# Kernel tuning notes

Hardware: AMD Instinct MI355X
Metric: run time of the kernel (lower is better)

## Reference

```python
import jax, jax.numpy as jnp
import numpy as np

N, C_IN, C_OUT, C_REL, T, V = 64, 256, 256, 32, 64, 25

def conv1x1(x, w, b):
    # x: (n, ci, a, b), w: (co, ci), b: (co,) -> (n, co, a, b)
    return jnp.einsum('oc,ncab->noab', w, x) + b[None, :, None, None]

def setup_inputs() -> dict:
    key = jax.random.key(0)
    ks = jax.random.split(key, 10)
    s_in = 1.0 / np.sqrt(C_IN)
    s_rel = 1.0 / np.sqrt(C_REL)
    return {
        'x': jax.random.normal(ks[0], (N, C_IN, T, V), dtype=jnp.float32),
        'A': jax.random.normal(ks[1], (V, V), dtype=jnp.float32),
        'w1': jax.random.uniform(ks[2], (C_REL, C_IN), jnp.float32, -s_in, s_in),
        'b1': jax.random.uniform(ks[3], (C_REL,), jnp.float32, -s_in, s_in),
        'w2': jax.random.uniform(ks[4], (C_REL, C_IN), jnp.float32, -s_in, s_in),
        'b2': jax.random.uniform(ks[5], (C_REL,), jnp.float32, -s_in, s_in),
        'w3': jax.random.uniform(ks[6], (C_OUT, C_IN), jnp.float32, -s_in, s_in),
        'b3': jax.random.uniform(ks[7], (C_OUT,), jnp.float32, -s_in, s_in),
        'w4': jax.random.uniform(ks[8], (C_OUT, C_REL), jnp.float32, -s_rel, s_rel),
        'b4': jax.random.uniform(ks[9], (C_OUT,), jnp.float32, -s_rel, s_rel),
        'threhold': 0,
        'alpha': 1,
    }

def reference(x, A, w1, b1, w2, b2, w3, b3, w4, b4, threhold, alpha):
    # x: (n, c, t, v)
    # pooled 1x1 convs: fold the T-mean before the channel mix (linear ops commute)
    xm = x.mean(-2)                                   # (n, c, v)
    x1 = jnp.einsum('oc,ncv->nov', w1, xm) + b1[None, :, None]   # (n, r, v)
    x2 = jnp.einsum('oc,ncv->nov', w2, xm) + b2[None, :, None]   # (n, r, v)
    x3 = conv1x1(x, w3, b3)                           # (n, co, t, v)
    # channel-wise affinity: outer difference + tanh -> (n, r, v, v)
    aff = jnp.tanh(x1[:, :, :, None] - x2[:, :, None, :])
    # 1x1 conv over rel channels, scale, add adjacency
    attn = jnp.einsum('or,nruv->nouv', w4, aff) + b4[None, :, None, None]
    attn = attn * alpha + A[None, None]               # (n, co, v, v)
    # graph conv contraction
    out = jnp.einsum('ncuv,nctu->nctv', attn, x3)     # (n, co, t, v)
    return out
```

## Files before the change

### kernel.cpp

```cpp
#include <hip/hip_runtime.h>

#define N_  64
#define CI  256
#define CO  256
#define CR  32
#define T_  64
#define V_  25
#define TV  (T_*V_)
#define VV  (V_*V_)
#define ATS 640

typedef __attribute__((ext_vector_type(8))) short bshort8;
typedef __attribute__((ext_vector_type(4))) float f32x4;

__device__ inline unsigned short f2bf(float f) {
    unsigned int u = __float_as_uint(f);
    return (unsigned short)((u + 0x7FFFu + ((u >> 16) & 1u)) >> 16);
}

__global__ __launch_bounds__(256) void k_mean_cvt(const float* __restrict__ x,
                                                  const float* __restrict__ w3,
                                                  const float* __restrict__ w4,
                                                  float* __restrict__ xm,
                                                  unsigned short* __restrict__ w3f,
                                                  unsigned short* __restrict__ w4f) {
    int b = blockIdx.x;
    int tid = threadIdx.x;
    if (b < 1024) {
        __shared__ float L[16 * 400];
        int n = b >> 4, c0 = (b & 15) * 16;
        float a0 = 0.f, a1 = 0.f;
        for (int ch = 0; ch < 4; ++ch) {
            for (int i = 0; i < 7; ++i) {
                int task = i * 256 + tid;
                if (task < 1600) {
                    int c = task / 100, f4 = task % 100;
                    *(float4*)&L[c * 400 + f4 * 4] =
                        *(const float4*)(x + (size_t)(n * CI + c0 + c) * TV + ch * 400 + f4 * 4);
                }
            }
            __syncthreads();
            {
                int c = tid / 25, v = tid % 25;
                float s = 0.f;
                #pragma unroll
                for (int tl = 0; tl < 16; ++tl) s += L[c * 400 + tl * 25 + v];
                a0 += s;
            }
            if (tid < 144) {
                int oi = tid + 256;
                int c = oi / 25, v = oi % 25;
                float s = 0.f;
                #pragma unroll
                for (int tl = 0; tl < 16; ++tl) s += L[c * 400 + tl * 25 + v];
                a1 += s;
            }
            __syncthreads();
        }
        xm[(size_t)(n * CI + c0) * V_ + tid] = a0 * (1.f / T_);
        if (tid < 144)
            xm[(size_t)(n * CI + c0) * V_ + tid + 256] = a1 * (1.f / T_);
    } else if (b < 1056) {
        int f = (b - 1024) * 256 + tid;
        int lane = f & 63;
        int ks = (f >> 6) & 7;
        int ot = f >> 9;
        const float* src = w3 + (size_t)(ot * 16 + (lane & 15)) * CI + ks * 32 + (lane >> 4) * 8;
        bshort8 v;
        #pragma unroll
        for (int i = 0; i < 8; ++i) v[i] = (short)f2bf(src[i]);
        *(bshort8*)(w3f + (size_t)f * 8) = v;
    } else {
        int f = (b - 1056) * 256 + tid;
        int lane = f & 63;
        int ot = f >> 6;
        const float* src = w4 + (size_t)(ot * 16 + (lane & 15)) * CR + (lane >> 4) * 8;
        bshort8 v;
        #pragma unroll
        for (int i = 0; i < 8; ++i) v[i] = (short)f2bf(src[i]);
        *(bshort8*)(w4f + (size_t)f * 8) = v;
    }
}

__global__ __launch_bounds__(256) void k_x1x2(const float* __restrict__ xm,
                                              const float* __restrict__ w1,
                                              const float* __restrict__ b1,
                                              const float* __restrict__ w2,
                                              const float* __restrict__ b2,
                                              float* __restrict__ x1,
                                              float* __restrict__ x2) {
    int n = blockIdx.x, q = blockIdx.y;
    __shared__ float s_xm[CI * V_];
    const float4* src = (const float4*)(xm + (size_t)n * CI * V_);
    for (int i = threadIdx.x; i < CI * V_ / 4; i += 256) ((float4*)s_xm)[i] = src[i];
    __syncthreads();
    if (threadIdx.x < 200) {
        int idx = q * 200 + threadIdx.x;
        int r = idx / V_, v = idx % V_;
        const float* wr1 = w1 + (size_t)r * CI;
        const float* wr2 = w2 + (size_t)r * CI;
        float p1a = 0.f, p1b = 0.f, p2a = 0.f, p2b = 0.f;
        #pragma unroll 4
        for (int c = 0; c < CI; c += 2) {
            float xv0 = s_xm[c * V_ + v];
            float xv1 = s_xm[(c + 1) * V_ + v];
            p1a += wr1[c] * xv0;  p1b += wr1[c + 1] * xv1;
            p2a += wr2[c] * xv0;  p2b += wr2[c + 1] * xv1;
        }
        x1[n * CR * V_ + idx] = p1a + p1b + b1[r];
        x2[n * CR * V_ + idx] = p2a + p2b + b2[r];
    }
}

__global__ __launch_bounds__(256) void k_attn_gemm(const float* __restrict__ x,
                                                   const unsigned short* __restrict__ w3f,
                                                   const float* __restrict__ b3,
                                                   unsigned short* __restrict__ x3,
                                                   const float* __restrict__ x1,
                                                   const float* __restrict__ x2,
                                                   const unsigned short* __restrict__ w4f,
                                                   const float* __restrict__ b4,
                                                   const float* __restrict__ A,
                                                   const int* __restrict__ alpha_p,
                                                   unsigned short* __restrict__ attnT) {
    __shared__ __align__(16) unsigned char smem[65536];
    int tid = threadIdx.x;
    int bb  = blockIdx.x;
    if (bb < 1600) {
        unsigned short* sB = (unsigned short*)smem;
        int n = bb / 25, j0 = (bb % 25) * 64;
        int lane = tid & 63, wave = tid >> 6;
        const float* gx = x + (size_t)n * CI * TV + j0;
        for (int i = 0; i < 16; ++i) {
            int task = i * 256 + tid;
            int c = task >> 4, chunk = task & 15;
            float4 v = *(const float4*)(gx + (size_t)c * TV + chunk * 4);
            int g0 = c >> 3, cl = c & 7;
            #pragma unroll
            for (int k = 0; k < 4; ++k) {
                int j = chunk * 4 + k;
                int f = g0 ^ (j & 7) ^ ((j >> 2) & 7);
                float val = (k == 0) ? v.x : (k == 1) ? v.y : (k == 2) ? v.z : v.w;
                sB[j * 256 + f * 8 + cl] = f2bf(val);
            }
        }
        __syncthreads();
        int quad = lane >> 4, c16 = lane & 15;
        const bshort8* Af = (const bshort8*)w3f;
        f32x4 acc[4][4];
        #pragma unroll
        for (int mt = 0; mt < 4; ++mt)
            #pragma unroll
            for (int nt = 0; nt < 4; ++nt) acc[mt][nt] = (f32x4){0,0,0,0};
        #pragma unroll
        for (int ks = 0; ks < 8; ++ks) {
            bshort8 b[4], a[4];
            #pragma unroll
            for (int nt = 0; nt < 4; ++nt) {
                int rB = nt * 16 + c16;
                int cidx = ks * 4 + quad;
                int f = cidx ^ (rB & 7) ^ ((rB >> 2) & 7);
                b[nt] = *(const bshort8*)(&sB[rB * 256 + f * 8]);
            }
            #pragma unroll
            for (int mt = 0; mt < 4; ++mt)
                a[mt] = Af[(size_t)(((wave * 4 + mt) * 8 + ks) * 64) + lane];
            #pragma unroll
            for (int mt = 0; mt < 4; ++mt)
                #pragma unroll
                for (int nt = 0; nt < 4; ++nt)
                    acc[mt][nt] = __builtin_amdgcn_mfma_f32_16x16x32_bf16(a[mt], b[nt], acc[mt][nt], 0, 0, 0);
        }
        __syncthreads();
        unsigned short* eS = sB;
        #pragma unroll
        for (int pass = 0; pass < 2; ++pass) {
            if ((wave >> 1) == pass) {
                #pragma unroll
                for (int mt = 0; mt < 4; ++mt) {
                    int o = wave * 64 + mt * 16 + quad * 4;
                    float4 bvv = *(const float4*)(b3 + o);
                    int ol = (wave & 1) * 64 + mt * 16 + quad * 4;
                    #pragma unroll
                    for (int nt = 0; nt < 4; ++nt) {
                        int jc = nt * 16 + c16;
                        eS[(ol + 0) * 72 + jc] = f2bf(acc[mt][nt][0] + bvv.x);
                        eS[(ol + 1) * 72 + jc] = f2bf(acc[mt][nt][1] + bvv.y);
                        eS[(ol + 2) * 72 + jc] = f2bf(acc[mt][nt][2] + bvv.z);
                        eS[(ol + 3) * 72 + jc] = f2bf(acc[mt][nt][3] + bvv.w);
                    }
                }
            }
            __syncthreads();
            #pragma unroll
            for (int i = 0; i < 4; ++i) {
                int task = i * 256 + tid;
                int orow = task >> 3, seg = task & 7;
                bshort8 vv = *(const bshort8*)&eS[orow * 72 + seg * 8];
                *(bshort8*)(x3 + (size_t)(n * CO + pass * 128 + orow) * TV + j0 + seg * 8) = vv;
            }
            __syncthreads();
        }
    } else {
        float* s_x1 = (float*)smem;
        float* s_x2 = s_x1 + CR * V_;
        float* s_A  = s_x2 + CR * V_;
        int b2 = bb - 1600;
        int n = b2 >> 3, by = b2 & 7;
        float alpha = (float)alpha_p[0];
        for (int i = tid; i < CR * V_; i += 256) {
            s_x1[i] = x1[n * CR * V_ + i];
            s_x2[i] = x2[n * CR * V_ + i];
        }
        for (int i = tid; i < VV; i += 256) s_A[i] = A[i];
        __syncthreads();
        int wave = tid >> 6, lane = tid & 63;
        int task = by * 4 + wave;
        int og   = task & 3;
        int ug   = task >> 2;
        int o0   = og * 64;
        int quad = lane >> 4, c16 = lane & 15;
        bshort8 a[4];
        #pragma unroll
        for (int ot = 0; ot < 4; ++ot)
            a[ot] = *(const bshort8*)(w4f + (size_t)(((og * 4) + ot) * 64 + lane) * 8);
        float4 bv[4];
        #pragma unroll
        for (int ot = 0; ot < 4; ++ot)
            bv[ot] = *(const float4*)(b4 + o0 + ot * 16 + quad * 4);
        int r0 = quad * 8;
        #pragma unroll
        for (int it = 0; it < 5; ++it) {
            int uv0 = (ug * 5 + it) * 16;
            int uvc = uv0 + c16;
            bool valid = uvc < VV;
            int uvcc = valid ? uvc : (VV - 1);
            int u = uvcc % V_, v = uvcc / V_;
            bshort8 b;
            #pragma unroll
            for (int i = 0; i < 8; ++i) {
                float d = s_x1[(r0 + i) * V_ + u] - s_x2[(r0 + i) * V_ + v];
                b[i] = (short)f2bf(tanhf(d));
            }
            float Auv = s_A[u * V_ + v];
            f32x4 acc[4];
            #pragma unroll
            for (int ot = 0; ot < 4; ++ot)
                acc[ot] = __builtin_amdgcn_mfma_f32_16x16x32_bf16(a[ot], b, (f32x4){0,0,0,0}, 0, 0, 0);
            if (valid) {
                #pragma unroll
                for (int ot = 0; ot < 4; ++ot) {
                    #pragma unroll
                    for (int r = 0; r < 4; ++r) {
                        int o = o0 + ot * 16 + quad * 4 + r;
                        float bval = (r == 0) ? bv[ot].x : (r == 1) ? bv[ot].y
                                   : (r == 2) ? bv[ot].z : bv[ot].w;
                        attnT[(size_t)(n * CO + o) * ATS + uvc] =
                            f2bf((acc[ot][r] + bval) * alpha + Auv);
                    }
                }
            }
        }
    }
}

__global__ __launch_bounds__(256) void k_contract(const unsigned short* __restrict__ x3,
                                                  const unsigned short* __restrict__ attnT,
                                                  float* __restrict__ out) {
    int no0 = blockIdx.x * 4;
    __shared__ __align__(16) unsigned short sB[4 * 1024];
    int tid = threadIdx.x;
    int p = tid >> 6, lane = tid & 63;
    int quad = lane >> 4, c16 = lane & 15;
    const unsigned short* pAg = x3 + (size_t)(no0 + p) * TV;
    bshort8 a[4];
    #pragma unroll
    for (int mt = 0; mt < 4; ++mt) {
        int t = mt * 16 + c16;
        const unsigned short* rowp = pAg + t * 25 + quad * 8;
        bshort8 av;
        #pragma unroll
        for (int i = 0; i < 8; ++i) {
            unsigned short val = rowp[i];
            av[i] = (short)((quad * 8 + i < 25) ? val : (unsigned short)0);
        }
        a[mt] = av;
    }
    {
        int task = tid;
        for (int i = 0; i < 3; ++i, task += 256)
            if (task < 700) {
                int pp = task / 175, rem = task % 175;
                sB[pp * 1024 + (rem / 7) * 32 + 25 + rem % 7] = 0;
            }
    }
    #pragma unroll
    for (int i = 0; i < 2; ++i) {
        int task = i * 256 + tid;
        if (task < 316) {
            int pp = task / 79, e8 = task % 79;
            bshort8 vv = *(const bshort8*)(attnT + (size_t)(no0 + pp) * ATS + e8 * 8);
            #pragma unroll
            for (int k = 0; k < 8; ++k) {
                int idx = e8 * 8 + k;
                if (idx < VV) {
                    int v = idx / 25, u = idx % 25;
                    sB[pp * 1024 + v * 32 + u] = (unsigned short)vv[k];
                }
            }
        }
    }
    __syncthreads();
    const unsigned short* pB = sB + p * 1024;
    bshort8 b[2];
    #pragma unroll
    for (int nt = 0; nt < 2; ++nt) b[nt] = *(const bshort8*)&pB[(nt * 16 + c16) * 32 + quad * 8];
    f32x4 acc[4][2];
    #pragma unroll
    for (int mt = 0; mt < 4; ++mt)
        #pragma unroll
        for (int nt = 0; nt < 2; ++nt)
            acc[mt][nt] = __builtin_amdgcn_mfma_f32_16x16x32_bf16(a[mt], b[nt], (f32x4){0,0,0,0}, 0, 0, 0);
    size_t ob = (size_t)(no0 + p) * TV;
    #pragma unroll
    for (int mt = 0; mt < 4; ++mt)
        #pragma unroll
        for (int nt = 0; nt < 2; ++nt) {
            int v = nt * 16 + c16;
            if (v < V_) {
                #pragma unroll
                for (int r = 0; r < 4; ++r) {
                    int t = mt * 16 + quad * 4 + r;
                    out[ob + t * 25 + v] = acc[mt][nt][r];
                }
            }
        }
}

extern "C" void kernel_launch(void* const* d_in, const int* in_sizes, int n_in,
                              void* d_out, int out_size, void* d_ws, size_t ws_size,
                              hipStream_t stream) {
    const float* x  = (const float*)d_in[0];
    const float* A  = (const float*)d_in[1];
    const float* w1 = (const float*)d_in[2];
    const float* b1 = (const float*)d_in[3];
    const float* w2 = (const float*)d_in[4];
    const float* b2 = (const float*)d_in[5];
    const float* w3 = (const float*)d_in[6];
    const float* b3 = (const float*)d_in[7];
    const float* w4 = (const float*)d_in[8];
    const float* b4 = (const float*)d_in[9];
    const int* alpha_p = (const int*)d_in[11];
    float* out = (float*)d_out;

    float* ws = (float*)d_ws;
    float* xm = ws;
    float* x1 = ws + 409600;
    float* x2 = ws + 460800;
    unsigned short* attnT = (unsigned short*)(ws + 512000);
    unsigned short* w3f   = attnT + (size_t)16384 * ATS;
    unsigned short* w4f   = w3f + 65536;
    unsigned short* x3    = w4f + 16384;

    k_mean_cvt<<<1060, 256, 0, stream>>>(x, w3, w4, xm, w3f, w4f);
    k_x1x2<<<dim3(N_, 4), 256, 0, stream>>>(xm, w1, b1, w2, b2, x1, x2);
    k_attn_gemm<<<2112, 256, 0, stream>>>(x, w3f, b3, x3, x1, x2, w4f, b4, A, alpha_p, attnT);
    k_contract<<<4096, 256, 0, stream>>>(x3, attnT, out);
}
```

Before: 293.8 us.

## Fuse x1/x2 projection into mean kernel via per-slice partial sums

Removes the separate k_x1x2 kernel. Each mean block now computes partial w1/w2 projections over its 16-channel slice and writes them out. The attention blocks of the GEMM kernel sum the 16 partials and add the biases. This saves one kernel launch and the xm round trip, at the cost of extra partial-sum traffic and a larger workspace.

```diff
diff --git a/kernel.cpp b/kernel.cpp
--- a/kernel.cpp
+++ b/kernel.cpp
@@ -21,14 +21,17 @@
 __global__ __launch_bounds__(256) void k_mean_cvt(const float* __restrict__ x,
                                                   const float* __restrict__ w3,
                                                   const float* __restrict__ w4,
-                                                  float* __restrict__ xm,
+                                                  const float* __restrict__ w1,
+                                                  const float* __restrict__ w2,
                                                   unsigned short* __restrict__ w3f,
-                                                  unsigned short* __restrict__ w4f) {
+                                                  unsigned short* __restrict__ w4f,
+                                                  float* __restrict__ part1,
+                                                  float* __restrict__ part2) {
     int b = blockIdx.x;
     int tid = threadIdx.x;
     if (b < 1024) {
         __shared__ float L[16 * 400];
-        int n = b >> 4, c0 = (b & 15) * 16;
+        int n = b >> 4, sl = b & 15, c0 = sl * 16;
         float a0 = 0.f, a1 = 0.f;
         for (int ch = 0; ch < 4; ++ch) {
             for (int i = 0; i < 7; ++i) {
@@ -57,9 +60,25 @@
             }
             __syncthreads();
         }
-        xm[(size_t)(n * CI + c0) * V_ + tid] = a0 * (1.f / T_);
-        if (tid < 144)
-            xm[(size_t)(n * CI + c0) * V_ + tid + 256] = a1 * (1.f / T_);
+        float* Lx = L;
+        Lx[tid] = a0 * (1.f / T_);
+        if (tid < 144) Lx[tid + 256] = a1 * (1.f / T_);
+        __syncthreads();
+        size_t pbase = ((size_t)n * 16 + sl) * 800;
+        for (int idx = tid; idx < CR * V_; idx += 256) {
+            int r = idx / V_, v = idx % V_;
+            const float* wr1 = w1 + (size_t)r * CI + c0;
+            const float* wr2 = w2 + (size_t)r * CI + c0;
+            float s1 = 0.f, s2 = 0.f;
+            #pragma unroll
+            for (int c = 0; c < 16; ++c) {
+                float xv = Lx[c * 25 + v];
+                s1 += wr1[c] * xv;
+                s2 += wr2[c] * xv;
+            }
+            part1[pbase + idx] = s1;
+            part2[pbase + idx] = s2;
+        }
     } else if (b < 1056) {
         int f = (b - 1024) * 256 + tid;
         int lane = f & 63;
@@ -82,42 +101,14 @@
     }
 }
 
-__global__ __launch_bounds__(256) void k_x1x2(const float* __restrict__ xm,
-                                              const float* __restrict__ w1,
-                                              const float* __restrict__ b1,
-                                              const float* __restrict__ w2,
-                                              const float* __restrict__ b2,
-                                              float* __restrict__ x1,
-                                              float* __restrict__ x2) {
-    int n = blockIdx.x, q = blockIdx.y;
-    __shared__ float s_xm[CI * V_];
-    const float4* src = (const float4*)(xm + (size_t)n * CI * V_);
-    for (int i = threadIdx.x; i < CI * V_ / 4; i += 256) ((float4*)s_xm)[i] = src[i];
-    __syncthreads();
-    if (threadIdx.x < 200) {
-        int idx = q * 200 + threadIdx.x;
-        int r = idx / V_, v = idx % V_;
-        const float* wr1 = w1 + (size_t)r * CI;
-        const float* wr2 = w2 + (size_t)r * CI;
-        float p1a = 0.f, p1b = 0.f, p2a = 0.f, p2b = 0.f;
-        #pragma unroll 4
-        for (int c = 0; c < CI; c += 2) {
-            float xv0 = s_xm[c * V_ + v];
-            float xv1 = s_xm[(c + 1) * V_ + v];
-            p1a += wr1[c] * xv0;  p1b += wr1[c + 1] * xv1;
-            p2a += wr2[c] * xv0;  p2b += wr2[c + 1] * xv1;
-        }
-        x1[n * CR * V_ + idx] = p1a + p1b + b1[r];
-        x2[n * CR * V_ + idx] = p2a + p2b + b2[r];
-    }
-}
-
 __global__ __launch_bounds__(256) void k_attn_gemm(const float* __restrict__ x,
                                                    const unsigned short* __restrict__ w3f,
                                                    const float* __restrict__ b3,
                                                    unsigned short* __restrict__ x3,
-                                                   const float* __restrict__ x1,
-                                                   const float* __restrict__ x2,
+                                                   const float* __restrict__ part1,
+                                                   const float* __restrict__ part2,
+                                                   const float* __restrict__ b1,
+                                                   const float* __restrict__ b2,
                                                    const unsigned short* __restrict__ w4f,
                                                    const float* __restrict__ b4,
                                                    const float* __restrict__ A,
@@ -205,12 +196,20 @@
         float* s_x1 = (float*)smem;
         float* s_x2 = s_x1 + CR * V_;
         float* s_A  = s_x2 + CR * V_;
-        int b2 = bb - 1600;
-        int n = b2 >> 3, by = b2 & 7;
+        int ib = bb - 1600;
+        int n = ib >> 3, by = ib & 7;
         float alpha = (float)alpha_p[0];
+        const float* pp1 = part1 + (size_t)n * 16 * 800;
+        const float* pp2 = part2 + (size_t)n * 16 * 800;
         for (int i = tid; i < CR * V_; i += 256) {
-            s_x1[i] = x1[n * CR * V_ + i];
-            s_x2[i] = x2[n * CR * V_ + i];
+            float s1 = b1[i / V_], s2 = b2[i / V_];
+            #pragma unroll
+            for (int s = 0; s < 16; ++s) {
+                s1 += pp1[s * 800 + i];
+                s2 += pp2[s * 800 + i];
+            }
+            s_x1[i] = s1;
+            s_x2[i] = s2;
         }
         for (int i = tid; i < VV; i += 256) s_A[i] = A[i];
         __syncthreads();
@@ -354,16 +353,14 @@
     float* out = (float*)d_out;
 
     float* ws = (float*)d_ws;
-    float* xm = ws;
-    float* x1 = ws + 409600;
-    float* x2 = ws + 460800;
-    unsigned short* attnT = (unsigned short*)(ws + 512000);
+    float* part1 = ws;
+    float* part2 = ws + 819200;
+    unsigned short* attnT = (unsigned short*)(ws + 1638400);
     unsigned short* w3f   = attnT + (size_t)16384 * ATS;
     unsigned short* w4f   = w3f + 65536;
     unsigned short* x3    = w4f + 16384;
 
-    k_mean_cvt<<<1060, 256, 0, stream>>>(x, w3, w4, xm, w3f, w4f);
-    k_x1x2<<<dim3(N_, 4), 256, 0, stream>>>(xm, w1, b1, w2, b2, x1, x2);
-    k_attn_gemm<<<2112, 256, 0, stream>>>(x, w3f, b3, x3, x1, x2, w4f, b4, A, alpha_p, attnT);
+    k_mean_cvt<<<1060, 256, 0, stream>>>(x, w3, w4, w1, w2, w3f, w4f, part1, part2);
+    k_attn_gemm<<<2112, 256, 0, stream>>>(x, w3f, b3, x3, part1, part2, b1, b2, w4f, b4, A, alpha_p, attnT);
     k_contract<<<4096, 256, 0, stream>>>(x3, attnT, out);
 }
```

Result: no change. 297.0 us (+1.1%).
